# Kernel optimization log

Measured on AMD Instinct MI355X. Metric: run time of the kernel, lower is better.

The kernel has to match this reference:

```python
import jax, jax.numpy as jnp
import numpy as np

K = 1024
D = 512
BETA = 0.25
ALPHA = 10.0
EPS_NORM = 1e-12  # torch F.normalize eps


def _l2_normalize(x):
    n = jnp.linalg.norm(x, axis=1, keepdims=True)
    return x / jnp.maximum(n, EPS_NORM)


def setup_inputs() -> dict:
    key = jax.random.key(0)
    k1, k2 = jax.random.split(key)
    latents = jax.random.normal(k1, (16384, D), dtype=jnp.float32)
    # nn.Embedding weight init: uniform(-1/K, 1/K)
    emb_weight = jax.random.uniform(k2, (K, D), dtype=jnp.float32,
                                    minval=-1.0 / K, maxval=1.0 / K)
    return {"latents": latents, "emb_weight": emb_weight}


def reference(latents, emb_weight):
    # latents: [B, D], emb_weight: [K, D]
    ln = _l2_normalize(latents)                               # [B, D]
    # torch uses embedding.weight.data -> detached for the attention path
    cb = _l2_normalize(jax.lax.stop_gradient(emb_weight))     # [K, D]
    attention = ln @ cb.T                                     # [B, K]
    soft_assign = jax.nn.softmax(ALPHA * attention, axis=1)   # [B, K]
    quantized = soft_assign @ emb_weight                      # [B, D]

    commitment_loss = jnp.mean((jax.lax.stop_gradient(quantized) - ln) ** 2)
    embedding_loss = jnp.mean((quantized - jax.lax.stop_gradient(ln)) ** 2)
    vq_loss = commitment_loss * BETA + embedding_loss

    avg_probs = jnp.mean(soft_assign, axis=0)                 # [K]
    entropy_vq = -jnp.sum(avg_probs * jnp.log(avg_probs + 1e-10))

    argm = jnp.argmax(attention, axis=1, keepdims=True)       # [B, 1] int
    one_hot = jax.nn.one_hot(argm[:, 0], K, dtype=latents.dtype)  # [B, K]
    hard_quantized = one_hot @ emb_weight                     # [B, D]
    # attention[one_hot.bool()].mean() == mean of row-max (argmax entries)
    cluster_metric = jnp.mean(jnp.max(attention, axis=1))

    return (quantized, vq_loss, entropy_vq, argm, hard_quantized,
            soft_assign, cluster_metric)
```

## Files before the change

kernel.cpp:

```cpp
#include <hip/hip_runtime.h>
#include <math.h>

#define D     512
#define KCB   1024
#define NT    256
#define NT2   512
#define RB    64
#define ALPHA 10.0f
#define TAU   0.008f
#define PSTR  1040

typedef __attribute__((ext_vector_type(8))) short short8v;
typedef __attribute__((ext_vector_type(4))) float f32x4;
typedef unsigned short us;

__device__ __forceinline__ float wave_reduce_sum(float v) {
    #pragma unroll
    for (int off = 32; off >= 1; off >>= 1) v += __shfl_xor(v, off, 64);
    return v;
}

__device__ __forceinline__ short bf16r(float x) {
    union { float f; unsigned u; } c; c.f = x;
    unsigned r = (c.u + 0x7FFFu + ((c.u >> 16) & 1u)) >> 16;
    return (short)r;
}

__global__ __launch_bounds__(NT) void k_prep2(const float* __restrict__ emb,
                                              us* __restrict__ cb, us* __restrict__ embT,
                                              float* __restrict__ cbinv,
                                              float* __restrict__ avg_ws,
                                              float* __restrict__ sse, float* __restrict__ clu) {
    const int k = blockIdx.x, t = threadIdx.x;
    const int wv = t >> 6, lane = t & 63;
    if (k < 4) avg_ws[k * NT + t] = 0.0f;
    if (k == 0 && t == 0) { *sse = 0.0f; *clu = 0.0f; }

    float2 v = ((const float2*)(emb + (size_t)k * D))[t];
    float ss = wave_reduce_sum(v.x * v.x + v.y * v.y);
    __shared__ float part[4];
    __shared__ float s_i;
    if (lane == 0) part[wv] = ss;
    __syncthreads();
    if (t == 0) s_i = 1.0f / fmaxf(sqrtf(part[0] + part[1] + part[2] + part[3]), 1e-12f);
    __syncthreads();
    float inv = s_i;
    const int d = 2 * t;
    unsigned lo = (unsigned short)bf16r(v.x * inv);
    unsigned hi = (unsigned short)bf16r(v.y * inv);
    size_t idx = (((size_t)(k >> 4) * 16 + (d >> 5)) * 64 + ((d >> 3) & 3) * 16 + (k & 15)) * 8 + (d & 7);
    ((unsigned*)cb)[idx >> 1] = lo | (hi << 16);
    size_t j0 = (((size_t)(d >> 4) * 32 + (k >> 5)) * 64 + ((k >> 3) & 3) * 16 + (d & 15)) * 8 + (k & 7);
    embT[j0]     = (us)bf16r(v.x);
    embT[j0 + 8] = (us)bf16r(v.y);
    if (t == 0) cbinv[k] = inv;
}

__global__ __launch_bounds__(NT2, 2) void k_fused(
    const float* __restrict__ lat, const float* __restrict__ emb,
    const us* __restrict__ cb, const us* __restrict__ embT, const float* __restrict__ cbinv,
    float* __restrict__ avg_ws, float* __restrict__ part_ws, int use_part,
    float* __restrict__ clu_ws, float* __restrict__ sse_ws,
    float* __restrict__ q_out, float* __restrict__ soft_out,
    float* __restrict__ argm_out, float* __restrict__ hq_out)
{
    extern __shared__ __align__(16) us pool[];
    __shared__ float s_inv[RB];
    __shared__ float s_maxp[8][RB];
    __shared__ float s_amax[RB];
    __shared__ float s_sump[8][RB];
    __shared__ float s_den[RB];
    __shared__ float s_bestv[RB];
    __shared__ int   s_besti[RB];
    __shared__ int   s_cnt;
    __shared__ int   s_ck[1024];
    __shared__ float s_cv[1024];
    __shared__ float part[8];

    const int t = threadIdx.x, wv = t >> 6, lane = t & 63;
    const int q15 = lane & 15, g = lane >> 4;
    const int b0 = blockIdx.x * RB;

    float4 ra[8], rb[8];
    #pragma unroll
    for (int i = 0; i < 8; ++i) {
        const float4* lp = (const float4*)(lat + (size_t)(b0 + wv * 8 + i) * D);
        ra[i] = lp[2 * lane]; rb[i] = lp[2 * lane + 1];
    }
    #pragma unroll
    for (int i = 0; i < 8; ++i) {
        int r = wv * 8 + i;
        float4 a = ra[i], b = rb[i];
        float ss = a.x*a.x + a.y*a.y + a.z*a.z + a.w*a.w
                 + b.x*b.x + b.y*b.y + b.z*b.z + b.w*b.w;
        ss = wave_reduce_sum(ss);
        float inv = 1.0f / fmaxf(sqrtf(ss), 1e-12f);
        short8v w;
        w[0] = bf16r(a.x * inv); w[1] = bf16r(a.y * inv);
        w[2] = bf16r(a.z * inv); w[3] = bf16r(a.w * inv);
        w[4] = bf16r(b.x * inv); w[5] = bf16r(b.y * inv);
        w[6] = bf16r(b.z * inv); w[7] = bf16r(b.w * inv);
        *(short8v*)&pool[(size_t)r * PSTR + lane * 8] = w;
        if (lane == 0) s_inv[r] = inv;
    }
    if (t == 0) s_cnt = 0;
    __syncthreads();

    f32x4 acc[4][8];
    #pragma unroll
    for (int m = 0; m < 4; ++m)
        #pragma unroll
        for (int ct = 0; ct < 8; ++ct) { f32x4 z = {0.f, 0.f, 0.f, 0.f}; acc[m][ct] = z; }

    const us* pBw = cb + (size_t)(wv * 8) * 16 * 512 + (size_t)lane * 8;
    #define LDB_A(ks, ct) (*(const short8v*)(pBw + (size_t)((ct) * 16 + (ks)) * 512))
    #define LDA_A(row, ks) (*(const short8v*)&pool[(size_t)(row) * PSTR + (ks) * 32 + g * 8])

    short8v bE[8], bO[8];
    #pragma unroll
    for (int ct = 0; ct < 8; ++ct) bE[ct] = LDB_A(0, ct);
    for (int ks = 0; ks < 16; ks += 2) {
        #pragma unroll
        for (int ct = 0; ct < 8; ++ct) bO[ct] = LDB_A(ks + 1, ct);
        {
            short8v af0 = LDA_A(q15, ks), af1 = LDA_A(16 + q15, ks);
            short8v af2 = LDA_A(32 + q15, ks), af3 = LDA_A(48 + q15, ks);
            #pragma unroll
            for (int ct = 0; ct < 8; ++ct) {
                acc[0][ct] = __builtin_amdgcn_mfma_f32_16x16x32_bf16(af0, bE[ct], acc[0][ct], 0, 0, 0);
                acc[1][ct] = __builtin_amdgcn_mfma_f32_16x16x32_bf16(af1, bE[ct], acc[1][ct], 0, 0, 0);
                acc[2][ct] = __builtin_amdgcn_mfma_f32_16x16x32_bf16(af2, bE[ct], acc[2][ct], 0, 0, 0);
                acc[3][ct] = __builtin_amdgcn_mfma_f32_16x16x32_bf16(af3, bE[ct], acc[3][ct], 0, 0, 0);
            }
        }
        const int ksn = (ks + 2 < 16) ? ks + 2 : 0;
        #pragma unroll
        for (int ct = 0; ct < 8; ++ct) bE[ct] = LDB_A(ksn, ct);
        {
            short8v af0 = LDA_A(q15, ks + 1), af1 = LDA_A(16 + q15, ks + 1);
            short8v af2 = LDA_A(32 + q15, ks + 1), af3 = LDA_A(48 + q15, ks + 1);
            #pragma unroll
            for (int ct = 0; ct < 8; ++ct) {
                acc[0][ct] = __builtin_amdgcn_mfma_f32_16x16x32_bf16(af0, bO[ct], acc[0][ct], 0, 0, 0);
                acc[1][ct] = __builtin_amdgcn_mfma_f32_16x16x32_bf16(af1, bO[ct], acc[1][ct], 0, 0, 0);
                acc[2][ct] = __builtin_amdgcn_mfma_f32_16x16x32_bf16(af2, bO[ct], acc[2][ct], 0, 0, 0);
                acc[3][ct] = __builtin_amdgcn_mfma_f32_16x16x32_bf16(af3, bO[ct], acc[3][ct], 0, 0, 0);
            }
        }
    }

    #pragma unroll
    for (int m = 0; m < 4; ++m)
        #pragma unroll
        for (int i = 0; i < 4; ++i) {
            float v = acc[m][0][i];
            #pragma unroll
            for (int ct = 1; ct < 8; ++ct) v = fmaxf(v, acc[m][ct][i]);
            #pragma unroll
            for (int off = 8; off >= 1; off >>= 1) v = fmaxf(v, __shfl_xor(v, off, 64));
            if (q15 == 0) s_maxp[wv][m * 16 + g * 4 + i] = v;
        }
    __syncthreads();
    if (t < RB) {
        float v = s_maxp[0][t];
        #pragma unroll
        for (int w = 1; w < 8; ++w) v = fmaxf(v, s_maxp[w][t]);
        s_amax[t] = v;
    }
    __syncthreads();

    #pragma unroll
    for (int m = 0; m < 4; ++m)
        #pragma unroll
        for (int i = 0; i < 4; ++i) {
            const int row = m * 16 + g * 4 + i;
            const float thr = s_amax[row] - TAU;
            #pragma unroll
            for (int ct = 0; ct < 8; ++ct) {
                if (acc[m][ct][i] >= thr) {
                    int idx = atomicAdd(&s_cnt, 1);
                    if (idx < 1024) s_ck[idx] = (row << 16) | (wv * 128 + ct * 16 + q15);
                }
            }
        }
    __syncthreads();
    const int cnt = (s_cnt < 1024) ? s_cnt : 1024;

    for (int e = wv; e < cnt; e += 8) {
        const int pk = s_ck[e];
        const int row = pk >> 16, kk = pk & 0xFFFF;
        const float4* lp = (const float4*)(lat + (size_t)(b0 + row) * D);
        const float4* ep = (const float4*)(emb + (size_t)kk * D);
        float4 x0 = lp[2 * lane], x1 = lp[2 * lane + 1];
        float4 y0 = ep[2 * lane], y1 = ep[2 * lane + 1];
        float dp = x0.x*y0.x + x0.y*y0.y + x0.z*y0.z + x0.w*y0.w
                 + x1.x*y1.x + x1.y*y1.y + x1.z*y1.z + x1.w*y1.w;
        dp = wave_reduce_sum(dp);
        if (lane == 0) s_cv[e] = dp * s_inv[row] * cbinv[kk];
    }
    __syncthreads();
    if (t < RB) {
        float bv = -1e30f; int bi = 0x7FFFFFFF;
        for (int e = 0; e < cnt; ++e) {
            if ((s_ck[e] >> 16) == t) {
                float v = s_cv[e]; int kk = s_ck[e] & 0xFFFF;
                if (v > bv || (v == bv && kk < bi)) { bv = v; bi = kk; }
            }
        }
        s_bestv[t] = bv; s_besti[t] = bi;
        argm_out[b0 + t] = (float)bi;
    }
    __syncthreads();

    #pragma unroll
    for (int m = 0; m < 4; ++m)
        #pragma unroll
        for (int i = 0; i < 4; ++i) {
            const float bvv = s_bestv[m * 16 + g * 4 + i];
            float s = 0.f;
            #pragma unroll
            for (int ct = 0; ct < 8; ++ct) {
                float e = __expf(ALPHA * (acc[m][ct][i] - bvv));
                acc[m][ct][i] = e;
                s += e;
            }
            #pragma unroll
            for (int off = 8; off >= 1; off >>= 1) s += __shfl_xor(s, off, 64);
            if (q15 == 0) s_sump[wv][m * 16 + g * 4 + i] = s;
        }
    __syncthreads();
    if (t < RB) {
        float s = s_sump[0][t];
        #pragma unroll
        for (int w = 1; w < 8; ++w) s += s_sump[w][t];
        s_den[t] = 1.0f / s;
    }
    __syncthreads();

    float csum[8];
    #pragma unroll
    for (int ct = 0; ct < 8; ++ct) csum[ct] = 0.f;
    #pragma unroll
    for (int m = 0; m < 4; ++m)
        #pragma unroll
        for (int i = 0; i < 4; ++i) {
            const int row = m * 16 + g * 4 + i;
            const float dn = s_den[row];
            float* orow = soft_out + (size_t)(b0 + row) * KCB + wv * 128 + q15;
            us* prow = &pool[(size_t)row * PSTR + wv * 128 + q15];
            #pragma unroll
            for (int ct = 0; ct < 8; ++ct) {
                float sv = acc[m][ct][i] * dn;
                orow[ct * 16] = sv;
                prow[ct * 16] = (us)bf16r(sv);
                csum[ct] += sv;
            }
        }
    #pragma unroll
    for (int ct = 0; ct < 8; ++ct) {
        float v = csum[ct];
        v += __shfl_xor(v, 16, 64);
        v += __shfl_xor(v, 32, 64);
        csum[ct] = v;
    }
    if (use_part) {
        if (lane < 16) {
            #pragma unroll
            for (int ct = 0; ct < 8; ++ct)
                part_ws[(size_t)blockIdx.x * KCB + wv * 128 + ct * 16 + lane] = csum[ct];
        }
    } else {
        if (lane < 16) {
            #pragma unroll
            for (int ct = 0; ct < 8; ++ct)
                atomicAdd(avg_ws + wv * 128 + ct * 16 + lane, csum[ct]);
        }
    }
    if (t == 0) {
        float cs = 0.f;
        #pragma unroll
        for (int r = 0; r < RB; ++r) cs += s_bestv[r];
        atomicAdd(clu_ws, cs);
    }
    __syncthreads();

    const float4* emb4 = (const float4*)emb;
    #pragma unroll
    for (int u = 0; u < 16; ++u) {
        int idx = t + u * NT2;
        int r = idx >> 7, c = idx & 127;
        ((float4*)(hq_out + (size_t)(b0 + r) * D))[c] = emb4[(size_t)s_besti[r] * 128 + c];
    }

    f32x4 qac[4][4];
    #pragma unroll
    for (int m = 0; m < 4; ++m)
        #pragma unroll
        for (int ct = 0; ct < 4; ++ct) { f32x4 z = {0.f, 0.f, 0.f, 0.f}; qac[m][ct] = z; }

    const us* pBq = embT + (size_t)(wv * 128) * 512 + (size_t)lane * 8;
    #define LDB_Q(ks, ct) (*(const short8v*)(pBq + (size_t)((ct) * 32 + (ks)) * 512))
    #define LDA_Q(row, ks) (*(const short8v*)&pool[(size_t)(row) * PSTR + (ks) * 32 + g * 8])

    short8v qE[4], qO[4];
    #pragma unroll
    for (int ct = 0; ct < 4; ++ct) qE[ct] = LDB_Q(0, ct);
    for (int ks = 0; ks < 32; ks += 2) {
        #pragma unroll
        for (int ct = 0; ct < 4; ++ct) qO[ct] = LDB_Q(ks + 1, ct);
        {
            short8v af0 = LDA_Q(q15, ks), af1 = LDA_Q(16 + q15, ks);
            short8v af2 = LDA_Q(32 + q15, ks), af3 = LDA_Q(48 + q15, ks);
            #pragma unroll
            for (int ct = 0; ct < 4; ++ct) {
                qac[0][ct] = __builtin_amdgcn_mfma_f32_16x16x32_bf16(af0, qE[ct], qac[0][ct], 0, 0, 0);
                qac[1][ct] = __builtin_amdgcn_mfma_f32_16x16x32_bf16(af1, qE[ct], qac[1][ct], 0, 0, 0);
                qac[2][ct] = __builtin_amdgcn_mfma_f32_16x16x32_bf16(af2, qE[ct], qac[2][ct], 0, 0, 0);
                qac[3][ct] = __builtin_amdgcn_mfma_f32_16x16x32_bf16(af3, qE[ct], qac[3][ct], 0, 0, 0);
            }
        }
        const int ksn = (ks + 2 < 32) ? ks + 2 : 0;
        #pragma unroll
        for (int ct = 0; ct < 4; ++ct) qE[ct] = LDB_Q(ksn, ct);
        {
            short8v af0 = LDA_Q(q15, ks + 1), af1 = LDA_Q(16 + q15, ks + 1);
            short8v af2 = LDA_Q(32 + q15, ks + 1), af3 = LDA_Q(48 + q15, ks + 1);
            #pragma unroll
            for (int ct = 0; ct < 4; ++ct) {
                qac[0][ct] = __builtin_amdgcn_mfma_f32_16x16x32_bf16(af0, qO[ct], qac[0][ct], 0, 0, 0);
                qac[1][ct] = __builtin_amdgcn_mfma_f32_16x16x32_bf16(af1, qO[ct], qac[1][ct], 0, 0, 0);
                qac[2][ct] = __builtin_amdgcn_mfma_f32_16x16x32_bf16(af2, qO[ct], qac[2][ct], 0, 0, 0);
                qac[3][ct] = __builtin_amdgcn_mfma_f32_16x16x32_bf16(af3, qO[ct], qac[3][ct], 0, 0, 0);
            }
        }
    }

    float sse = 0.f;
    #pragma unroll
    for (int m = 0; m < 4; ++m)
        #pragma unroll
        for (int i = 0; i < 4; ++i) {
            const int rloc = m * 16 + g * 4 + i;
            const int row = b0 + rloc;
            const float rv = s_inv[rloc];
            const float* lrow = lat + (size_t)row * D + wv * 64 + q15;
            float* qrow = q_out + (size_t)row * D + wv * 64 + q15;
            #pragma unroll
            for (int ct = 0; ct < 4; ++ct) {
                float qv = qac[m][ct][i];
                qrow[ct * 16] = qv;
                float df = qv - lrow[ct * 16] * rv;
                sse += df * df;
            }
        }
    sse = wave_reduce_sum(sse);
    if (lane == 0) part[wv] = sse;
    __syncthreads();
    if (t == 0) {
        float s = 0.f;
        #pragma unroll
        for (int w = 0; w < 8; ++w) s += part[w];
        atomicAdd(sse_ws, s);
    }
    #undef LDB_A
    #undef LDA_A
    #undef LDB_Q
    #undef LDA_Q
}

__global__ __launch_bounds__(NT) void k_avg(const float* __restrict__ part_ws, float* __restrict__ avg_ws,
                                            int nblk) {
    const int c  = (blockIdx.x & 3) * NT + threadIdx.x;
    const int r0 = (blockIdx.x >> 2) * (nblk / 4);
    const int r1 = r0 + nblk / 4;
    float s = 0.f;
    for (int r = r0; r < r1; ++r) s += part_ws[(size_t)r * KCB + c];
    atomicAdd(avg_ws + c, s);
}

__global__ __launch_bounds__(NT) void k_final(
    const float* __restrict__ avg_ws, const float* __restrict__ sse_ws, const float* __restrict__ clu_ws,
    float* __restrict__ out_vq, float* __restrict__ out_ent, float* __restrict__ out_cm,
    float invB, float invBD)
{
    const int t = threadIdx.x;
    float ent = 0.f;
    for (int idx = t; idx < KCB; idx += NT) {
        float pv = avg_ws[idx] * invB;
        ent -= pv * logf(pv + 1e-10f);
    }
    ent = wave_reduce_sum(ent);
    __shared__ float part[4];
    const int wv = t >> 6, lane = t & 63;
    if (lane == 0) part[wv] = ent;
    __syncthreads();
    if (t == 0) {
        *out_ent = part[0] + part[1] + part[2] + part[3];
        *out_vq  = 1.25f * (*sse_ws) * invBD;
        *out_cm  = (*clu_ws) * invB;
    }
}

extern "C" void kernel_launch(void* const* d_in, const int* in_sizes, int n_in,
                              void* d_out, int out_size, void* d_ws, size_t ws_size,
                              hipStream_t stream)
{
    const float* lat = (const float*)d_in[0];
    const float* emb = (const float*)d_in[1];
    const int B = in_sizes[0] / D;
    float* out = (float*)d_out;

    const size_t vq_off   = (size_t)B * D;
    const size_t ent_off  = vq_off + 1;
    const size_t argm_off = vq_off + 2;
    const size_t hq_off   = argm_off + (size_t)B;
    const size_t soft_off = hq_off + (size_t)B * D;
    const size_t cm_off   = soft_off + (size_t)B * KCB;

    const int nblk = B / RB;

    us* cb_bf   = (us*)d_ws;
    us* embT_bf = cb_bf + (size_t)KCB * D;
    float* fbase  = (float*)(embT_bf + (size_t)D * KCB);
    float* cbinv  = fbase;
    float* avg_ws = cbinv + KCB;
    float* sse_ws = avg_ws + KCB;
    float* clu_ws = sse_ws + 1;
    float* part_ws = clu_ws + 1;

    const size_t base_bytes = (size_t)((char*)part_ws - (char*)d_ws);
    const int use_part = (ws_size >= base_bytes + (size_t)nblk * KCB * 4) ? 1 : 0;

    const int lds_bytes = RB * PSTR * 2;

    k_prep2<<<KCB, NT, 0, stream>>>(emb, cb_bf, embT_bf, cbinv, avg_ws, sse_ws, clu_ws);
    k_fused<<<nblk, NT2, lds_bytes, stream>>>(lat, emb, cb_bf, embT_bf, cbinv,
                                              avg_ws, part_ws, use_part, clu_ws, sse_ws,
                                              out, out + soft_off, out + argm_off, out + hq_off);
    if (use_part) k_avg<<<16, NT, 0, stream>>>(part_ws, avg_ws, nblk);
    k_final<<<1, NT, 0, stream>>>(avg_ws, sse_ws, clu_ws,
                                  out + vq_off, out + ent_off, out + cm_off,
                                  1.0f / (float)B, 1.0f / ((float)B * (float)D));
}
```

Before: 277.3 us.

## Fuse prep, main, and reduction kernels into one persistent kernel with grid barriers

Merges the codebook prep kernel, the fused attention/softmax kernel, and the avg/final reduction kernels into a single launch that uses atomic-counter grid barriers between phases. Codebook normalization and bf16 retiling are done by 64 blocks through an LDS tile, which gives coalesced stores to the swizzled layouts. The goal is to remove the launch gaps and tail effects of four separate kernels. In exchange every block spins at a grid barrier, which is only safe if all 256 blocks are co-resident (2 per CU), and a memset is now issued before the launch.

```diff
diff --git a/kernel.cpp b/kernel.cpp
--- a/kernel.cpp
+++ b/kernel.cpp
@@ -3,7 +3,6 @@
 
 #define D     512
 #define KCB   1024
-#define NT    256
 #define NT2   512
 #define RB    64
 #define ALPHA 10.0f
@@ -26,43 +25,31 @@
     return (short)r;
 }
 
-__global__ __launch_bounds__(NT) void k_prep2(const float* __restrict__ emb,
-                                              us* __restrict__ cb, us* __restrict__ embT,
-                                              float* __restrict__ cbinv,
-                                              float* __restrict__ avg_ws,
-                                              float* __restrict__ sse, float* __restrict__ clu) {
-    const int k = blockIdx.x, t = threadIdx.x;
-    const int wv = t >> 6, lane = t & 63;
-    if (k < 4) avg_ws[k * NT + t] = 0.0f;
-    if (k == 0 && t == 0) { *sse = 0.0f; *clu = 0.0f; }
-
-    float2 v = ((const float2*)(emb + (size_t)k * D))[t];
-    float ss = wave_reduce_sum(v.x * v.x + v.y * v.y);
-    __shared__ float part[4];
-    __shared__ float s_i;
-    if (lane == 0) part[wv] = ss;
-    __syncthreads();
-    if (t == 0) s_i = 1.0f / fmaxf(sqrtf(part[0] + part[1] + part[2] + part[3]), 1e-12f);
-    __syncthreads();
-    float inv = s_i;
-    const int d = 2 * t;
-    unsigned lo = (unsigned short)bf16r(v.x * inv);
-    unsigned hi = (unsigned short)bf16r(v.y * inv);
-    size_t idx = (((size_t)(k >> 4) * 16 + (d >> 5)) * 64 + ((d >> 3) & 3) * 16 + (k & 15)) * 8 + (d & 7);
-    ((unsigned*)cb)[idx >> 1] = lo | (hi << 16);
-    size_t j0 = (((size_t)(d >> 4) * 32 + (k >> 5)) * 64 + ((k >> 3) & 3) * 16 + (d & 15)) * 8 + (k & 7);
-    embT[j0]     = (us)bf16r(v.x);
-    embT[j0 + 8] = (us)bf16r(v.y);
-    if (t == 0) cbinv[k] = inv;
+__device__ __forceinline__ void gbar_arrive(int* c) {
+    __syncthreads();
+    if (threadIdx.x == 0) {
+        __threadfence();
+        __hip_atomic_fetch_add(c, 1, __ATOMIC_RELEASE, __HIP_MEMORY_SCOPE_AGENT);
+    }
 }
-
-__global__ __launch_bounds__(NT2, 2) void k_fused(
+__device__ __forceinline__ void gbar_wait(int* c, int tgt) {
+    if (threadIdx.x == 0) {
+        while (__hip_atomic_load(c, __ATOMIC_ACQUIRE, __HIP_MEMORY_SCOPE_AGENT) < tgt)
+            __builtin_amdgcn_s_sleep(4);
+        __threadfence();
+    }
+    __syncthreads();
+}
+
+__global__ __launch_bounds__(NT2, 2) void k_all(
     const float* __restrict__ lat, const float* __restrict__ emb,
-    const us* __restrict__ cb, const us* __restrict__ embT, const float* __restrict__ cbinv,
-    float* __restrict__ avg_ws, float* __restrict__ part_ws, int use_part,
-    float* __restrict__ clu_ws, float* __restrict__ sse_ws,
+    us* __restrict__ cb, us* __restrict__ embT, float* __restrict__ cbinv,
+    float* __restrict__ avg_ws, float* __restrict__ scal,
+    float* __restrict__ part_ws, float* __restrict__ red_ws, int use_part,
     float* __restrict__ q_out, float* __restrict__ soft_out,
-    float* __restrict__ argm_out, float* __restrict__ hq_out)
+    float* __restrict__ argm_out, float* __restrict__ hq_out,
+    float* __restrict__ out_vq, float* __restrict__ out_ent, float* __restrict__ out_cm,
+    float invB, float invBD, int nblk)
 {
     extern __shared__ __align__(16) us pool[];
     __shared__ float s_inv[RB];
@@ -79,7 +66,60 @@
 
     const int t = threadIdx.x, wv = t >> 6, lane = t & 63;
     const int q15 = lane & 15, g = lane >> 4;
-    const int b0 = blockIdx.x * RB;
+    const int bid = blockIdx.x;
+    const int b0 = bid * RB;
+
+    float* sse_ws = scal;
+    float* clu_ws = scal + 1;
+    int*   ctr    = (int*)(scal + 2);
+
+    if (bid < 64) {
+        us* tileN = pool;
+        us* tileR = pool + 16 * 512;
+        const int kg = bid;
+        #pragma unroll
+        for (int rr = 0; rr < 2; ++rr) {
+            const int kk = wv * 2 + rr;
+            const int k = kg * 16 + kk;
+            const float4* ep = (const float4*)(emb + (size_t)k * D);
+            float4 a = ep[2 * lane], b = ep[2 * lane + 1];
+            float ss = a.x*a.x + a.y*a.y + a.z*a.z + a.w*a.w
+                     + b.x*b.x + b.y*b.y + b.z*b.z + b.w*b.w;
+            ss = wave_reduce_sum(ss);
+            float inv = 1.0f / fmaxf(sqrtf(ss), 1e-12f);
+            short8v wn, wr;
+            wn[0] = bf16r(a.x * inv); wn[1] = bf16r(a.y * inv);
+            wn[2] = bf16r(a.z * inv); wn[3] = bf16r(a.w * inv);
+            wn[4] = bf16r(b.x * inv); wn[5] = bf16r(b.y * inv);
+            wn[6] = bf16r(b.z * inv); wn[7] = bf16r(b.w * inv);
+            wr[0] = bf16r(a.x); wr[1] = bf16r(a.y); wr[2] = bf16r(a.z); wr[3] = bf16r(a.w);
+            wr[4] = bf16r(b.x); wr[5] = bf16r(b.y); wr[6] = bf16r(b.z); wr[7] = bf16r(b.w);
+            *(short8v*)&tileN[(size_t)kk * 512 + lane * 8] = wn;
+            *(short8v*)&tileR[(size_t)kk * 512 + lane * 8] = wr;
+            if (lane == 0) cbinv[k] = inv;
+        }
+        __syncthreads();
+        #pragma unroll
+        for (int u = 0; u < 2; ++u) {
+            int ch = t + u * NT2;
+            int k15 = ch & 15, j4 = (ch >> 4) & 3, c = ch >> 6;
+            short8v w = *(short8v*)&tileN[(size_t)k15 * 512 + c * 32 + j4 * 8];
+            *(short8v*)(cb + (size_t)kg * 8192 + (size_t)ch * 8) = w;
+        }
+        const int kc = kg >> 1, khalf = kg & 1;
+        #pragma unroll
+        for (int u = 0; u < 2; ++u) {
+            int ch = t + u * NT2;
+            int dc = ch >> 5, cc = ch & 31, hb = cc >> 4, dl = cc & 15;
+            int dd = dc * 16 + dl;
+            short8v w;
+            #pragma unroll
+            for (int j = 0; j < 8; ++j) w[j] = (short)tileR[(size_t)(hb * 8 + j) * 512 + dd];
+            *(short8v*)(embT + ((size_t)(dc * 32 + kc)) * 512 + khalf * 256 + (size_t)cc * 8) = w;
+        }
+    }
+    gbar_arrive(&ctr[0]);
+    gbar_wait(&ctr[0], nblk);
 
     float4 ra[8], rb[8];
     #pragma unroll
@@ -267,7 +307,7 @@
         if (lane < 16) {
             #pragma unroll
             for (int ct = 0; ct < 8; ++ct)
-                part_ws[(size_t)blockIdx.x * KCB + wv * 128 + ct * 16 + lane] = csum[ct];
+                part_ws[(size_t)bid * KCB + wv * 128 + ct * 16 + lane] = csum[ct];
         }
     } else {
         if (lane < 16) {
@@ -366,38 +406,61 @@
     #undef LDA_A
     #undef LDB_Q
     #undef LDA_Q
-}
-
-__global__ __launch_bounds__(NT) void k_avg(const float* __restrict__ part_ws, float* __restrict__ avg_ws,
-                                            int nblk) {
-    const int c  = (blockIdx.x & 3) * NT + threadIdx.x;
-    const int r0 = (blockIdx.x >> 2) * (nblk / 4);
-    const int r1 = r0 + nblk / 4;
-    float s = 0.f;
-    for (int r = r0; r < r1; ++r) s += part_ws[(size_t)r * KCB + c];
-    atomicAdd(avg_ws + c, s);
-}
-
-__global__ __launch_bounds__(NT) void k_final(
-    const float* __restrict__ avg_ws, const float* __restrict__ sse_ws, const float* __restrict__ clu_ws,
-    float* __restrict__ out_vq, float* __restrict__ out_ent, float* __restrict__ out_cm,
-    float invB, float invBD)
-{
-    const int t = threadIdx.x;
-    float ent = 0.f;
-    for (int idx = t; idx < KCB; idx += NT) {
-        float pv = avg_ws[idx] * invB;
-        ent -= pv * logf(pv + 1e-10f);
-    }
-    ent = wave_reduce_sum(ent);
-    __shared__ float part[4];
-    const int wv = t >> 6, lane = t & 63;
-    if (lane == 0) part[wv] = ent;
-    __syncthreads();
-    if (t == 0) {
-        *out_ent = part[0] + part[1] + part[2] + part[3];
-        *out_vq  = 1.25f * (*sse_ws) * invBD;
-        *out_cm  = (*clu_ws) * invB;
+
+    gbar_arrive(&ctr[1]);
+    if (use_part) {
+        if (bid < 16) {
+            gbar_wait(&ctr[1], nblk);
+            for (int c = t; c < KCB; c += NT2) {
+                float s = 0.f;
+                #pragma unroll
+                for (int r = 0; r < 16; ++r) s += part_ws[(size_t)(bid * 16 + r) * KCB + c];
+                red_ws[(size_t)bid * KCB + c] = s;
+            }
+            gbar_arrive(&ctr[2]);
+            if (bid == 0) {
+                gbar_wait(&ctr[2], 16);
+                float ent = 0.f;
+                for (int c = t; c < KCB; c += NT2) {
+                    float av = 0.f;
+                    #pragma unroll
+                    for (int j = 0; j < 16; ++j) av += red_ws[(size_t)j * KCB + c];
+                    float pv = av * invB;
+                    ent -= pv * logf(pv + 1e-10f);
+                }
+                ent = wave_reduce_sum(ent);
+                if (lane == 0) part[wv] = ent;
+                __syncthreads();
+                if (t == 0) {
+                    float e = 0.f;
+                    #pragma unroll
+                    for (int w = 0; w < 8; ++w) e += part[w];
+                    *out_ent = e;
+                    *out_vq  = 1.25f * (*sse_ws) * invBD;
+                    *out_cm  = (*clu_ws) * invB;
+                }
+            }
+        }
+    } else {
+        if (bid == 0) {
+            gbar_wait(&ctr[1], nblk);
+            float ent = 0.f;
+            for (int c = t; c < KCB; c += NT2) {
+                float pv = avg_ws[c] * invB;
+                ent -= pv * logf(pv + 1e-10f);
+            }
+            ent = wave_reduce_sum(ent);
+            if (lane == 0) part[wv] = ent;
+            __syncthreads();
+            if (t == 0) {
+                float e = 0.f;
+                #pragma unroll
+                for (int w = 0; w < 8; ++w) e += part[w];
+                *out_ent = e;
+                *out_vq  = 1.25f * (*sse_ws) * invBD;
+                *out_cm  = (*clu_ws) * invB;
+            }
+        }
     }
 }
 
@@ -419,26 +482,25 @@
 
     const int nblk = B / RB;
 
-    us* cb_bf   = (us*)d_ws;
-    us* embT_bf = cb_bf + (size_t)KCB * D;
-    float* fbase  = (float*)(embT_bf + (size_t)D * KCB);
-    float* cbinv  = fbase;
+    us* cb_bf    = (us*)d_ws;
+    us* embT_bf  = cb_bf + (size_t)KCB * D;
+    float* cbinv = (float*)(embT_bf + (size_t)D * KCB);
     float* avg_ws = cbinv + KCB;
-    float* sse_ws = avg_ws + KCB;
-    float* clu_ws = sse_ws + 1;
-    float* part_ws = clu_ws + 1;
-
-    const size_t base_bytes = (size_t)((char*)part_ws - (char*)d_ws);
-    const int use_part = (ws_size >= base_bytes + (size_t)nblk * KCB * 4) ? 1 : 0;
+    float* scal   = avg_ws + KCB;
+    float* part_ws = scal + 8;
+    float* red_ws  = part_ws + (size_t)nblk * KCB;
+
+    const size_t need = (size_t)((char*)(red_ws + 16 * KCB) - (char*)d_ws);
+    const int use_part = (ws_size >= need) ? 1 : 0;
+
+    if (use_part) hipMemsetAsync(scal, 0, 32, stream);
+    else          hipMemsetAsync(avg_ws, 0, KCB * 4 + 32, stream);
 
     const int lds_bytes = RB * PSTR * 2;
 
-    k_prep2<<<KCB, NT, 0, stream>>>(emb, cb_bf, embT_bf, cbinv, avg_ws, sse_ws, clu_ws);
-    k_fused<<<nblk, NT2, lds_bytes, stream>>>(lat, emb, cb_bf, embT_bf, cbinv,
-                                              avg_ws, part_ws, use_part, clu_ws, sse_ws,
-                                              out, out + soft_off, out + argm_off, out + hq_off);
-    if (use_part) k_avg<<<16, NT, 0, stream>>>(part_ws, avg_ws, nblk);
-    k_final<<<1, NT, 0, stream>>>(avg_ws, sse_ws, clu_ws,
-                                  out + vq_off, out + ent_off, out + cm_off,
-                                  1.0f / (float)B, 1.0f / ((float)B * (float)D));
+    k_all<<<nblk, NT2, lds_bytes, stream>>>(lat, emb, cb_bf, embT_bf, cbinv,
+                                            avg_ws, scal, part_ws, red_ws, use_part,
+                                            out, out + soft_off, out + argm_off, out + hq_off,
+                                            out + vq_off, out + ent_off, out + cm_off,
+                                            1.0f / (float)B, 1.0f / ((float)B * (float)D), nblk);
 }
```

After: 304.8 us. +9.9%, slower.
